# Kernel tuning notes

Hardware: AMD Instinct MI355X
Metric: run time of the kernel (lower is better)

## Reference

```python
import math
import jax, jax.numpy as jnp
import numpy as np

EPS = 1e-5

def lstm(x, Wih, Whh, b):
    # x: [N,T,D]; PyTorch gate order i,f,g,o; b = b_ih + b_hh combined
    N = x.shape[0]
    H = Whh.shape[1]
    gx = jnp.einsum('ntd,gd->ntg', x, Wih) + b  # [N,T,4H]
    def step(carry, g):
        h, c = carry
        z = g + h @ Whh.T
        i, f, gg, o = jnp.split(z, 4, axis=-1)
        c = jax.nn.sigmoid(f) * c + jax.nn.sigmoid(i) * jnp.tanh(gg)
        h = jax.nn.sigmoid(o) * jnp.tanh(c)
        return (h, c), h
    init = (jnp.zeros((N, H), x.dtype), jnp.zeros((N, H), x.dtype))
    (hN, _), ys = jax.lax.scan(step, init, jnp.swapaxes(gx, 0, 1))
    return jnp.swapaxes(ys, 0, 1), hN  # outputs [N,T,H], h_n [N,H]

def bilstm_layer(x, fW, fU, fb, bW, bU, bb):
    of, _ = lstm(x, fW, fU, fb)
    ob, _ = lstm(x[:, ::-1], bW, bU, bb)
    return jnp.concatenate([of, ob[:, ::-1]], axis=-1)

def layernorm(x, g, b):
    m = jnp.mean(x, -1, keepdims=True)
    v = jnp.mean((x - m) ** 2, -1, keepdims=True)
    return (x - m) * jax.lax.rsqrt(v + EPS) * g + b

def encoder_layer(src, Wq, bq, Wk, bk, Wv, bv, Wo, bo, W1, b1, W2, b2, lng, lnb):
    B, S, d = src.shape
    G, NH = 5, 5
    dk = d // NH
    # group channel shuffle (as in source)
    qs = src.reshape(B, S, G, d // G).swapaxes(-1, -2).reshape(B, S, d)
    q = qs @ Wq.T + bq
    k = q @ Wk.T + bk   # NOTE: source applies W_k/W_v to the projected query
    v = q @ Wv.T + bv
    def heads(t):
        return t.reshape(B, S, NH, dk).transpose(0, 2, 1, 3)
    qh, kh, vh = heads(q), heads(k), heads(v)
    attn = jax.nn.softmax(jnp.einsum('bhqd,bhkd->bhqk', qh, kh) / math.sqrt(dk), axis=-1)
    o = jnp.einsum('bhqk,bhkd->bhqd', attn, vh).transpose(0, 2, 1, 3).reshape(B, S, d)
    o = o @ Wo.T + bo
    src = layernorm(src + o, lng, lnb)          # dropout is identity in eval
    ff = jax.nn.relu(src @ W1.T + b1) @ W2.T + b2
    src = layernorm(src + ff, lng, lnb)         # same LayerNorm params reused
    return src, attn

def _forward(x, qWih, qWhh, qb, kWih, kWhh, kb, vWih, vWhh, vb,
             tWq, tbq, tWk, tbk, tWv, tbv, tWo, tbo, tW1, tb1, tW2, tb2, tlng, tlnb,
             l0fWih, l0fWhh, l0fb, l0bWih, l0bWhh, l0bb,
             l1fWih, l1fWhh, l1fb, l1bWih, l1bWhh, l1bb,
             fc1W, fc1b, fc2W, fc2b):
    B, T, F = x.shape
    H = qWhh.shape[1]
    # per-feature LSTMs: shared weights across features -> batch them
    xf = x.transpose(0, 2, 1).reshape(B * F, T, 1)
    _, hq = lstm(xf, qWih, qWhh, qb)   # [B*F,H]
    _, hk = lstm(xf, kWih, kWhh, kb)   # [B*F,H]
    _, hv = lstm(xf, vWih, vWhh, vb)   # [B*F,1]
    Q = hq.reshape(B, F, H)
    K = hk.reshape(B, F, H)
    V = hv.reshape(B, F)
    # b_ij = (q_i . k_j)/sqrt(H) * v_j, softmax over j
    scores = jnp.einsum('bih,bjh->bij', Q, K) / math.sqrt(H) * V[:, None, :]
    Wsm = jax.nn.softmax(scores, axis=-1)          # [B,F,F] rows indexed by i
    attn_output = jnp.einsum('btj,bij->bti', x, Wsm)  # bmm(x, softmax_b_i)
    b = Wsm.transpose(0, 2, 1)                     # stack(b_list, dim=-1)
    src = jnp.concatenate([x, attn_output], axis=-1)  # [B,T,2F]
    attns = []
    for l in range(2):
        src, a = encoder_layer(src, tWq[l], tbq[l], tWk[l], tbk[l], tWv[l], tbv[l],
                               tWo[l], tbo[l], tW1[l], tb1[l], tW2[l], tb2[l],
                               tlng[l], tlnb[l])
        attns.append(a)
    c = jnp.stack(attns)                           # [2,B,5,T,T]
    out = bilstm_layer(src, l0fWih, l0fWhh, l0fb, l0bWih, l0bWhh, l0bb)
    out = bilstm_layer(out, l1fWih, l1fWhh, l1fb, l1bWih, l1bWhh, l1bb)
    out = jax.nn.relu(out[:, -1, :])               # [B,2H]
    out = jax.nn.relu(out @ fc1W.T + fc1b)
    out = out @ fc2W.T + fc2b                      # [B,1]
    return out, b, c

def setup_inputs() -> dict:
    B, T, F, H = 16, 128, 40, 64
    d = 2 * F
    key = jax.random.key(0)
    ks = iter(jax.random.split(key, 64))
    def n(shape, fan):
        return (jax.random.normal(next(ks), shape) / math.sqrt(fan)).astype(jnp.float32)
    inp = {'x': jax.random.normal(next(ks), (B, T, F), dtype=jnp.float32)}
    # per-feature LSTMs
    inp.update(qWih=n((4 * H, 1), 1), qWhh=n((4 * H, H), H), qb=n((4 * H,), H))
    inp.update(kWih=n((4 * H, 1), 1), kWhh=n((4 * H, H), H), kb=n((4 * H,), H))
    inp.update(vWih=n((4, 1), 1), vWhh=n((4, 1), 1), vb=n((4,), 1))
    # transformer (2 layers stacked on leading axis)
    inp.update(tWq=n((2, d, d), d), tbq=n((2, d), d), tWk=n((2, d, d), d), tbk=n((2, d), d),
               tWv=n((2, d, d), d), tbv=n((2, d), d), tWo=n((2, d, d), d), tbo=n((2, d), d),
               tW1=n((2, 4 * d, d), d), tb1=n((2, 4 * d), d), tW2=n((2, d, 4 * d), 4 * d),
               tb2=n((2, d), 4 * d), tlng=jnp.ones((2, d), jnp.float32), tlnb=jnp.zeros((2, d), jnp.float32))
    # main bidirectional 2-layer LSTM
    inp.update(l0fWih=n((4 * H, d), d), l0fWhh=n((4 * H, H), H), l0fb=n((4 * H,), H),
               l0bWih=n((4 * H, d), d), l0bWhh=n((4 * H, H), H), l0bb=n((4 * H,), H),
               l1fWih=n((4 * H, 2 * H), 2 * H), l1fWhh=n((4 * H, H), H), l1fb=n((4 * H,), H),
               l1bWih=n((4 * H, 2 * H), 2 * H), l1bWhh=n((4 * H, H), H), l1bb=n((4 * H,), H))
    inp.update(fc1W=n((H, 2 * H), 2 * H), fc1b=n((H,), 2 * H), fc2W=n((1, H), H), fc2b=n((1,), H))
    return inp

def reference(x, qWih, qWhh, qb, kWih, kWhh, kb, vWih, vWhh, vb,
              tWq, tbq, tWk, tbk, tWv, tbv, tWo, tbo, tW1, tb1, tW2, tb2, tlng, tlnb,
              l0fWih, l0fWhh, l0fb, l0bWih, l0bWhh, l0bb,
              l1fWih, l1fWhh, l1fb, l1bWih, l1bWhh, l1bb,
              fc1W, fc1b, fc2W, fc2b):
    return _forward(x, qWih, qWhh, qb, kWih, kWhh, kb, vWih, vWhh, vb,
                    tWq, tbq, tWk, tbk, tWv, tbv, tWo, tbo, tW1, tb1, tW2, tb2, tlng, tlnb,
                    l0fWih, l0fWhh, l0fb, l0bWih, l0bWhh, l0bb,
                    l1fWih, l1fWhh, l1fb, l1bWih, l1bWhh, l1bb,
                    fc1W, fc1b, fc2W, fc2b)
```

## Files before the change

kernel.cpp:

```cpp
#include <hip/hip_runtime.h>

__device__ __forceinline__ float sigf(float x){ return 1.0f/(1.0f+__expf(-x)); }
__device__ __forceinline__ float tanhfast(float x){ return 1.0f - 2.0f/(__expf(2.0f*x)+1.0f); }

#define Bn 16
#define Tn 128
#define Fn 40
#define Hn 64
#define Dn 80
#define NHn 5
#define DKn 16
#define FFn 320

#define LOAD_PIN_ROW(dst, srcp)                                        \
  {                                                                    \
    _Pragma("unroll")                                                  \
    for (int jj=0; jj<16; ++jj){                                       \
      float4 tv = *(const float4*)((srcp) + 4*jj);                     \
      dst[4*jj]=tv.x; dst[4*jj+1]=tv.y; dst[4*jj+2]=tv.z; dst[4*jj+3]=tv.w; \
    }                                                                  \
    _Pragma("unroll")                                                  \
    for (int jj=0; jj<64; ++jj){ asm volatile("" : "+v"(dst[jj])); }   \
  }

#define LD4(p,i) (((const float4*)(p))[i])
#define DECL8(v, p) \
  float4 v##0=LD4(p,0), v##1=LD4(p,1), v##2=LD4(p,2), v##3=LD4(p,3), \
         v##4=LD4(p,4), v##5=LD4(p,5), v##6=LD4(p,6), v##7=LD4(p,7);
#define PIN4(P) asm volatile("" : "+v"(P.x), "+v"(P.y), "+v"(P.z), "+v"(P.w));
#define PIN8(v) PIN4(v##0) PIN4(v##1) PIN4(v##2) PIN4(v##3) PIN4(v##4) PIN4(v##5) \
  PIN4(v##6) PIN4(v##7)
#define ACC8(base) \
  { const float4 h0=hb4[(base)+0]; a += h0.x*w0.x + h0.y*w0.y + h0.z*w0.z + h0.w*w0.w; } \
  { const float4 h1=hb4[(base)+1]; a += h1.x*w1.x + h1.y*w1.y + h1.z*w1.z + h1.w*w1.w; } \
  { const float4 h2=hb4[(base)+2]; a += h2.x*w2.x + h2.y*w2.y + h2.z*w2.z + h2.w*w2.w; } \
  { const float4 h3=hb4[(base)+3]; a += h3.x*w3.x + h3.y*w3.y + h3.z*w3.z + h3.w*w3.w; } \
  { const float4 h4=hb4[(base)+4]; a += h4.x*w4.x + h4.y*w4.y + h4.z*w4.z + h4.w*w4.w; } \
  { const float4 h5=hb4[(base)+5]; a += h5.x*w5.x + h5.y*w5.y + h5.z*w5.z + h5.w*w5.w; } \
  { const float4 h6=hb4[(base)+6]; a += h6.x*w6.x + h6.y*w6.y + h6.z*w6.z + h6.w*w6.w; } \
  { const float4 h7=hb4[(base)+7]; a += h7.x*w7.x + h7.y*w7.y + h7.z*w7.z + h7.w*w7.w; }

__global__ __launch_bounds__(128,1) void k_feat_lstm2(
    const float* __restrict__ x,
    const float* __restrict__ qWih, const float* __restrict__ qWhh, const float* __restrict__ qb,
    const float* __restrict__ kWih, const float* __restrict__ kWhh, const float* __restrict__ kb,
    const float* __restrict__ vWih, const float* __restrict__ vWhh, const float* __restrict__ vb,
    float* __restrict__ hq, float* __restrict__ hk, float* __restrict__ hv)
{
  const int blk = blockIdx.x;
  const int l = threadIdx.x;
  if (blk >= 1280){
    const int inst = (blk - 1280)*128 + l;
    const int bi = inst/Fn, f = inst%Fn;
    const float* xp = x + bi*Tn*Fn + f;
    const float wih0=vWih[0], wih1=vWih[1], wih2=vWih[2], wih3=vWih[3];
    const float u0=vWhh[0], u1=vWhh[1], u2=vWhh[2], u3=vWhh[3];
    const float c0=vb[0], c1=vb[1], c2=vb[2], c3=vb[3];
    float h=0.f, c=0.f;
    #pragma unroll 1
    for (int t=0;t<Tn;++t){
      float xt = xp[t*Fn];
      float zi = xt*wih0 + h*u0 + c0;
      float zf = xt*wih1 + h*u1 + c1;
      float zg = xt*wih2 + h*u2 + c2;
      float zo = xt*wih3 + h*u3 + c3;
      c = sigf(zf)*c + sigf(zi)*tanhfast(zg);
      h = sigf(zo)*tanhfast(c);
    }
    hv[inst] = h;
    return;
  }
  const bool isk = blk >= 640;
  const int inst = isk ? blk-640 : blk;
  const int bi = inst/Fn, f = inst%Fn;
  const float* Whh = isk ? kWhh : qWhh;
  const float* Wih = isk ? kWih : qWih;
  const float* bia = isk ? kb  : qb;
  float* outp = isk ? hk : hq;

  const int r0 = l;
  const int r1 = l + 128;

  float w0[Hn], w1[Hn];
  LOAD_PIN_ROW(w0, Whh + r0*Hn);
  LOAD_PIN_ROW(w1, Whh + r1*Hn);
  const float wih0 = Wih[r0], wih1 = Wih[r1];
  const float bb0 = bia[r0], bb1 = bia[r1];

  __shared__ __align__(16) float hb[Hn];
  __shared__ float zb[4*Hn];
  __shared__ float xls[Tn];

  const float* xp = x + bi*Tn*Fn + f;
  xls[l] = xp[l*Fn];
  if (l < Hn) hb[l] = 0.f;
  float c = 0.f, h = 0.f;
  __syncthreads();

  const float4* hb4 = (const float4*)hb;
  #pragma unroll 1
  for (int t=0;t<Tn;++t){
    const float xt = xls[t];
    float a0 = bb0 + xt*wih0;
    float a1 = bb1 + xt*wih1;
    #pragma unroll
    for (int jj=0; jj<16; ++jj){
      const float4 hv4 = hb4[jj];
      a0 += hv4.x*w0[4*jj  ] + hv4.y*w0[4*jj+1] + hv4.z*w0[4*jj+2] + hv4.w*w0[4*jj+3];
      a1 += hv4.x*w1[4*jj  ] + hv4.y*w1[4*jj+1] + hv4.z*w1[4*jj+2] + hv4.w*w1[4*jj+3];
    }
    if (l >= Hn){ zb[l] = a0; zb[l+128] = a1; }
    __syncthreads();
    if (l < Hn){
      const float zi = a0, zg = a1;
      const float zf = zb[l+64], zo = zb[l+192];
      c = sigf(zf)*c + sigf(zi)*tanhfast(zg);
      h = sigf(zo)*tanhfast(c);
      hb[l] = h;
    }
    __syncthreads();
  }
  if (l < Hn) outp[inst*Hn + l] = h;
}

__global__ __launch_bounds__(64) void k_featattn(
    const float* __restrict__ hq, const float* __restrict__ hk, const float* __restrict__ hv,
    float* __restrict__ Wsm, float* __restrict__ out_b)
{
  const int blk = blockIdx.x;
  const int bi = blk / Fn, i = blk % Fn;
  const int j = threadIdx.x;
  __shared__ float qrow[Hn];
  qrow[j] = hq[blk*Hn + j];
  __syncthreads();
  float s = -1e30f;
  if (j < Fn){
    const float* krow = hk + (bi*Fn + j)*Hn;
    float a = 0.f;
    #pragma unroll
    for (int h2=0; h2<Hn; ++h2) a += qrow[h2]*krow[h2];
    s = a * 0.125f * hv[bi*Fn + j];
  }
  float m = s;
  #pragma unroll
  for (int off=32; off>0; off>>=1) m = fmaxf(m, __shfl_xor(m, off));
  float e = (j < Fn) ? __expf(s - m) : 0.f;
  float tot = e;
  #pragma unroll
  for (int off=32; off>0; off>>=1) tot += __shfl_xor(tot, off);
  float p = e / tot;
  if (j < Fn){
    Wsm[blk*Fn + j] = p;
    out_b[bi*(Fn*Fn) + j*Fn + i] = p;
  }
}

__global__ __launch_bounds__(128) void k_build_src(
    const float* __restrict__ x, const float* __restrict__ Wsm, float* __restrict__ src)
{
  const int blk = blockIdx.x;
  const int bi = blk / Tn;
  const int tid = threadIdx.x;
  __shared__ float xrow[Fn];
  if (tid < Fn) xrow[tid] = x[blk*Fn + tid];
  __syncthreads();
  if (tid < Fn){
    src[blk*Dn + tid] = xrow[tid];
  } else if (tid < Dn){
    const int i = tid - Fn;
    const float* wrow = Wsm + (bi*Fn + i)*Fn;
    float a = 0.f;
    #pragma unroll
    for (int j2=0;j2<Fn;++j2) a += xrow[j2]*wrow[j2];
    src[blk*Dn + tid] = a;
  }
}

__global__ __launch_bounds__(128) void k_qkv(
    const float* __restrict__ src,
    const float* __restrict__ Wq, const float* __restrict__ bq,
    const float* __restrict__ Wk, const float* __restrict__ bk,
    const float* __restrict__ Wv, const float* __restrict__ bv,
    float* __restrict__ q, float* __restrict__ k, float* __restrict__ v)
{
  const int row = blockIdx.x;
  const int t = threadIdx.x;
  __shared__ float qs[Dn];
  __shared__ float qrow[Dn];
  if (t < Dn) qs[t] = src[row*Dn + (t%5)*16 + t/5];
  __syncthreads();
  if (t < Dn){
    const float* wr = Wq + t*Dn;
    float a = bq[t];
    #pragma unroll 8
    for (int d2=0; d2<Dn; ++d2) a += qs[d2]*wr[d2];
    qrow[t] = a;
    q[row*Dn + t] = a;
  }
  __syncthreads();
  if (t < Dn){
    const float* wk = Wk + t*Dn;
    const float* wv = Wv + t*Dn;
    float ak = bk[t], av = bv[t];
    #pragma unroll 8
    for (int d2=0; d2<Dn; ++d2){ float qq = qrow[d2]; ak += qq*wk[d2]; av += qq*wv[d2]; }
    k[row*Dn + t] = ak;
    v[row*Dn + t] = av;
  }
}

__global__ __launch_bounds__(128) void k_attn(
    const float* __restrict__ q, const float* __restrict__ k, const float* __restrict__ v,
    float* __restrict__ o, float* __restrict__ c_out)
{
  const int s1 = blockIdx.x, h = blockIdx.y, bi = blockIdx.z;
  const int s2 = threadIdx.x;
  __shared__ float qf[DKn];
  __shared__ float p[Tn];
  __shared__ float pa[128];
  __shared__ float red_m[2];
  __shared__ float red_s[2];
  if (s2 < DKn) qf[s2] = q[(bi*Tn + s1)*Dn + h*DKn + s2];
  __syncthreads();
  const float* krow = k + (bi*Tn + s2)*Dn + h*DKn;
  float a = 0.f;
  #pragma unroll
  for (int d2=0; d2<DKn; ++d2) a += qf[d2]*krow[d2];
  a *= 0.25f;
  const int wv_id = s2 >> 6;
  float m = a;
  #pragma unroll
  for (int off=32; off>0; off>>=1) m = fmaxf(m, __shfl_xor(m, off));
  if ((s2 & 63) == 0) red_m[wv_id] = m;
  __syncthreads();
  m = fmaxf(red_m[0], red_m[1]);
  float e = __expf(a - m);
  float tot = e;
  #pragma unroll
  for (int off=32; off>0; off>>=1) tot += __shfl_xor(tot, off);
  if ((s2 & 63) == 0) red_s[wv_id] = tot;
  __syncthreads();
  tot = red_s[0] + red_s[1];
  float pv = e / tot;
  p[s2] = pv;
  c_out[((bi*NHn + h)*Tn + s1)*Tn + s2] = pv;
  __syncthreads();
  {
    const int d    = s2 & 15;
    const int part = s2 >> 4;
    const float* vcol = v + bi*Tn*Dn + h*DKn + d;
    float acc = 0.f;
    #pragma unroll
    for (int jj=0; jj<16; ++jj){
      const int j2 = part*16 + jj;
      acc += p[j2]*vcol[j2*Dn];
    }
    pa[s2] = acc;
  }
  __syncthreads();
  if (s2 < DKn){
    float acc = 0.f;
    #pragma unroll
    for (int k2=0; k2<8; ++k2) acc += pa[k2*16 + s2];
    o[(bi*Tn + s1)*Dn + h*DKn + s2] = acc;
  }
}

__global__ __launch_bounds__(320) void k_oln_ffln(
    const float* __restrict__ o, const float* __restrict__ Wo, const float* __restrict__ bo,
    const float* __restrict__ W1, const float* __restrict__ b1,
    const float* __restrict__ W2, const float* __restrict__ b2,
    const float* __restrict__ lng, const float* __restrict__ lnb, float* __restrict__ src)
{
  const int row = blockIdx.x;
  const int t = threadIdx.x;
  __shared__ float orow[Dn];
  __shared__ float s1row[Dn];
  __shared__ float h1[FFn];
  __shared__ float red[128];
  if (t < Dn) orow[t] = o[row*Dn + t];
  __syncthreads();
  float val = 0.f;
  if (t < Dn){
    const float* wr = Wo + t*Dn;
    float a = bo[t];
    #pragma unroll 8
    for (int d2=0; d2<Dn; ++d2) a += orow[d2]*wr[d2];
    val = a + src[row*Dn + t];
  }
  if (t < 128) red[t] = (t < Dn) ? val : 0.f;
  __syncthreads();
  for (int s=64; s>0; s>>=1){ if (t < s) red[t] += red[t+s]; __syncthreads(); }
  float mean = red[0] * (1.f/Dn);
  __syncthreads();
  if (t < 128){ float dv = (t < Dn) ? (val - mean) : 0.f; red[t] = dv*dv; }
  __syncthreads();
  for (int s=64; s>0; s>>=1){ if (t < s) red[t] += red[t+s]; __syncthreads(); }
  float rstd = rsqrtf(red[0]*(1.f/Dn) + 1e-5f);
  if (t < Dn) s1row[t] = (val - mean)*rstd*lng[t] + lnb[t];
  __syncthreads();
  {
    const float* wr = W1 + t*Dn;
    float a = b1[t];
    #pragma unroll 8
    for (int d2=0; d2<Dn; ++d2) a += s1row[d2]*wr[d2];
    h1[t] = fmaxf(a, 0.f);
  }
  __syncthreads();
  float val2 = 0.f;
  if (t < Dn){
    const float* wr = W2 + t*FFn;
    float a = b2[t];
    #pragma unroll 8
    for (int d2=0; d2<FFn; ++d2) a += h1[d2]*wr[d2];
    val2 = a + s1row[t];
  }
  if (t < 128) red[t] = (t < Dn) ? val2 : 0.f;
  __syncthreads();
  for (int s=64; s>0; s>>=1){ if (t < s) red[t] += red[t+s]; __syncthreads(); }
  mean = red[0] * (1.f/Dn);
  __syncthreads();
  if (t < 128){ float dv = (t < Dn) ? (val2 - mean) : 0.f; red[t] = dv*dv; }
  __syncthreads();
  for (int s=64; s>0; s>>=1){ if (t < s) red[t] += red[t+s]; __syncthreads(); }
  rstd = rsqrtf(red[0]*(1.f/Dn) + 1e-5f);
  if (t < Dn) src[row*Dn + t] = (val2 - mean)*rstd*lng[t] + lnb[t];
}

template<int IND>
__global__ __launch_bounds__(256) void k_gx8(
    const float* __restrict__ X,
    const float* __restrict__ WihF, const float* __restrict__ bF,
    const float* __restrict__ WihB, const float* __restrict__ bB,
    float* __restrict__ gx)
{
  const int row0 = blockIdx.x * 8;
  const int dir = blockIdx.y;
  const int g = threadIdx.x;
  __shared__ float xs[8][IND];
  #pragma unroll
  for (int rr=0; rr<8; ++rr)
    for (int d2=g; d2<IND; d2+=256) xs[rr][d2] = X[(row0+rr)*IND + d2];
  __syncthreads();
  const float* W  = dir ? WihB : WihF;
  const float* bb = dir ? bB  : bF;
  const float* wr = W + g*IND;
  float acc[8];
  const float b0 = bb[g];
  #pragma unroll
  for (int rr=0; rr<8; ++rr) acc[rr] = b0;
  #pragma unroll 4
  for (int d2=0; d2<IND; d2+=4){
    const float4 wv = *(const float4*)(wr + d2);
    #pragma unroll
    for (int rr=0; rr<8; ++rr){
      acc[rr] += xs[rr][d2]*wv.x + xs[rr][d2+1]*wv.y + xs[rr][d2+2]*wv.z + xs[rr][d2+3]*wv.w;
    }
  }
  float* gxd = gx + dir*(Bn*Tn*256);
  #pragma unroll
  for (int rr=0; rr<8; ++rr) gxd[(row0+rr)*256 + g] = acc[rr];
}

__global__ __launch_bounds__(512)
void k_bilstm_rec5(
    const float* __restrict__ gx,
    const float* __restrict__ WhhF, const float* __restrict__ WhhB,
    float* __restrict__ outp)
{
  const int n = blockIdx.x;
  const int dir = blockIdx.y;
  const int t = threadIdx.x;
  const int half = t >> 8;
  const int r    = t & 255;
  const float* Whh = dir ? WhhB : WhhF;
  DECL8(w, Whh + r*Hn + half*32);
  PIN8(w);

  __shared__ __align__(16) float hb[Hn];
  __shared__ float pa[512];
  if (t < Hn) hb[t] = 0.f;
  float c = 0.f, h = 0.f;
  __syncthreads();

  const float* gxd = gx + dir*(Bn*Tn*256) + n*Tn*256;
  const float4* hb4 = (const float4*)hb;
  const int jbase = half*8;
  const int t0 = dir ? Tn-1 : 0;
  float g0 = half ? 0.f : gxd[t0*256 + r];
  #pragma unroll 1
  for (int step=0; step<Tn; ++step){
    const int tt = dir ? (Tn-1-step) : step;
    int tn = dir ? (Tn-2-step) : (step+1);
    tn = max(0, min(Tn-1, tn));
    const float p0 = half ? 0.f : gxd[tn*256 + r];
    float a = g0;
    ACC8(jbase)
    pa[t] = a;
    __syncthreads();
    if (t < Hn){
      const float zi = pa[t    ] + pa[t+256];
      const float zf = pa[t+ 64] + pa[t+320];
      const float zg = pa[t+128] + pa[t+384];
      const float zo = pa[t+192] + pa[t+448];
      c = sigf(zf)*c + sigf(zi)*tanhfast(zg);
      h = sigf(zo)*tanhfast(c);
      hb[t] = h;
      outp[(n*Tn + tt)*128 + dir*Hn + t] = h;
    }
    __syncthreads();
    g0 = p0;
  }
}

__global__ __launch_bounds__(128) void k_final(
    const float* __restrict__ out1,
    const float* __restrict__ fc1W, const float* __restrict__ fc1b,
    const float* __restrict__ fc2W, const float* __restrict__ fc2b,
    float* __restrict__ outp)
{
  const int n = blockIdx.x;
  const int t = threadIdx.x;
  __shared__ float r[128];
  __shared__ float a1[64];
  r[t] = fmaxf(out1[(n*Tn + (Tn-1))*128 + t], 0.f);
  __syncthreads();
  if (t < 64){
    const float* wr = fc1W + t*128;
    float a = fc1b[t];
    #pragma unroll 8
    for (int d2=0; d2<128; ++d2) a += r[d2]*wr[d2];
    a1[t] = fmaxf(a, 0.f);
  }
  __syncthreads();
  if (t == 0){
    float a = fc2b[0];
    #pragma unroll 8
    for (int d2=0; d2<64; ++d2) a += a1[d2]*fc2W[d2];
    outp[n] = a;
  }
}

extern "C" void kernel_launch(void* const* d_in, const int* in_sizes, int n_in,
                              void* d_out, int out_size, void* d_ws, size_t ws_size,
                              hipStream_t stream)
{
  const float* x     = (const float*)d_in[0];
  const float* qWih  = (const float*)d_in[1];
  const float* qWhh  = (const float*)d_in[2];
  const float* qb    = (const float*)d_in[3];
  const float* kWih  = (const float*)d_in[4];
  const float* kWhh  = (const float*)d_in[5];
  const float* kb    = (const float*)d_in[6];
  const float* vWih  = (const float*)d_in[7];
  const float* vWhh  = (const float*)d_in[8];
  const float* vb    = (const float*)d_in[9];
  const float* tWq   = (const float*)d_in[10];
  const float* tbq   = (const float*)d_in[11];
  const float* tWk   = (const float*)d_in[12];
  const float* tbk   = (const float*)d_in[13];
  const float* tWv   = (const float*)d_in[14];
  const float* tbv   = (const float*)d_in[15];
  const float* tWo   = (const float*)d_in[16];
  const float* tbo   = (const float*)d_in[17];
  const float* tW1   = (const float*)d_in[18];
  const float* tb1   = (const float*)d_in[19];
  const float* tW2   = (const float*)d_in[20];
  const float* tb2   = (const float*)d_in[21];
  const float* tlng  = (const float*)d_in[22];
  const float* tlnb  = (const float*)d_in[23];
  const float* l0fWih= (const float*)d_in[24];
  const float* l0fWhh= (const float*)d_in[25];
  const float* l0fb  = (const float*)d_in[26];
  const float* l0bWih= (const float*)d_in[27];
  const float* l0bWhh= (const float*)d_in[28];
  const float* l0bb  = (const float*)d_in[29];
  const float* l1fWih= (const float*)d_in[30];
  const float* l1fWhh= (const float*)d_in[31];
  const float* l1fb  = (const float*)d_in[32];
  const float* l1bWih= (const float*)d_in[33];
  const float* l1bWhh= (const float*)d_in[34];
  const float* l1bb  = (const float*)d_in[35];
  const float* fc1W  = (const float*)d_in[36];
  const float* fc1b  = (const float*)d_in[37];
  const float* fc2W  = (const float*)d_in[38];
  const float* fc2b  = (const float*)d_in[39];

  float* ws  = (float*)d_ws;
  float* hq  = ws;
  float* hk  = hq  + 640*64;
  float* hv  = hk  + 640*64;
  float* Wsm = hv  + 640;
  float* src = Wsm + 16*40*40;
  float* q   = src + 16*128*80;
  float* k   = q   + 16*128*80;
  float* v   = k   + 16*128*80;
  float* o   = v   + 16*128*80;
  float* gx  = o   + 16*128*80;
  float* lout0 = gx + 2*16*128*256;
  float* lout1 = lout0 + 16*128*128;

  float* outp  = (float*)d_out;
  float* out_b = outp + 16;
  float* out_c = out_b + 16*40*40;

  k_feat_lstm2<<<1285, 128, 0, stream>>>(x, qWih,qWhh,qb, kWih,kWhh,kb, vWih,vWhh,vb, hq,hk,hv);
  k_featattn<<<640, 64, 0, stream>>>(hq, hk, hv, Wsm, out_b);
  k_build_src<<<2048, 128, 0, stream>>>(x, Wsm, src);
  for (int l=0; l<2; ++l){
    k_qkv<<<2048, 128, 0, stream>>>(src, tWq + l*Dn*Dn, tbq + l*Dn,
                                    tWk + l*Dn*Dn, tbk + l*Dn,
                                    tWv + l*Dn*Dn, tbv + l*Dn, q, k, v);
    k_attn<<<dim3(128,5,16), 128, 0, stream>>>(q, k, v, o, out_c + (size_t)l*16*5*128*128);
    k_oln_ffln<<<2048, 320, 0, stream>>>(o, tWo + l*Dn*Dn, tbo + l*Dn,
                                         tW1 + l*FFn*Dn, tb1 + l*FFn,
                                         tW2 + l*Dn*FFn, tb2 + l*Dn,
                                         tlng + l*Dn, tlnb + l*Dn, src);
  }
  k_gx8<80><<<dim3(256,2), 256, 0, stream>>>(src, l0fWih, l0fb, l0bWih, l0bb, gx);
  k_bilstm_rec5<<<dim3(16,2), 512, 0, stream>>>(gx, l0fWhh, l0bWhh, lout0);
  k_gx8<128><<<dim3(256,2), 256, 0, stream>>>(lout0, l1fWih, l1fb, l1bWih, l1bb, gx);
  k_bilstm_rec5<<<dim3(16,2), 512, 0, stream>>>(gx, l1fWhh, l1bWhh, lout1);
  k_final<<<16, 128, 0, stream>>>(lout1, fc1W, fc1b, fc2W, fc2b, outp);
}
```

Baseline: 665.3 us.

## Use one gate row per thread in feature LSTM with 256-thread blocks

The per-feature LSTM kernel now uses 256 threads per block, each holding one 64-wide Whh row in registers instead of two. All gate pre-activations go through shared memory, and the dot product is split into two accumulators for more instruction-level parallelism. Launch bounds allow five blocks per CU, cutting register pressure and raising occupancy. The scalar v-LSTM tail now packs 256 instances per block. The trade-off is twice as many threads taking part in each step's barriers.

```diff
diff --git a/kernel.cpp b/kernel.cpp
--- a/kernel.cpp
+++ b/kernel.cpp
@@ -11,17 +11,6 @@
 #define NHn 5
 #define DKn 16
 #define FFn 320
-
-#define LOAD_PIN_ROW(dst, srcp)                                        \
-  {                                                                    \
-    _Pragma("unroll")                                                  \
-    for (int jj=0; jj<16; ++jj){                                       \
-      float4 tv = *(const float4*)((srcp) + 4*jj);                     \
-      dst[4*jj]=tv.x; dst[4*jj+1]=tv.y; dst[4*jj+2]=tv.z; dst[4*jj+3]=tv.w; \
-    }                                                                  \
-    _Pragma("unroll")                                                  \
-    for (int jj=0; jj<64; ++jj){ asm volatile("" : "+v"(dst[jj])); }   \
-  }
 
 #define LD4(p,i) (((const float4*)(p))[i])
 #define DECL8(v, p) \
@@ -40,7 +29,15 @@
   { const float4 h6=hb4[(base)+6]; a += h6.x*w6.x + h6.y*w6.y + h6.z*w6.z + h6.w*w6.w; } \
   { const float4 h7=hb4[(base)+7]; a += h7.x*w7.x + h7.y*w7.y + h7.z*w7.z + h7.w*w7.w; }
 
-__global__ __launch_bounds__(128,1) void k_feat_lstm2(
+#define CAT_(a,b) a##b
+#define CAT(a,b) CAT_(a,b)
+#define ACC1P(v, n, idx, acc) \
+  { const float4 hh=hb4[(idx)]; acc += hh.x*CAT(v,n).x + hh.y*CAT(v,n).y + hh.z*CAT(v,n).z + hh.w*CAT(v,n).w; }
+#define ACC8P(v, base, acc) \
+  ACC1P(v,0,(base)+0,acc) ACC1P(v,1,(base)+1,acc) ACC1P(v,2,(base)+2,acc) ACC1P(v,3,(base)+3,acc) \
+  ACC1P(v,4,(base)+4,acc) ACC1P(v,5,(base)+5,acc) ACC1P(v,6,(base)+6,acc) ACC1P(v,7,(base)+7,acc)
+
+__global__ __launch_bounds__(256,5) void k_feat_lstm2(
     const float* __restrict__ x,
     const float* __restrict__ qWih, const float* __restrict__ qWhh, const float* __restrict__ qb,
     const float* __restrict__ kWih, const float* __restrict__ kWhh, const float* __restrict__ kb,
@@ -50,7 +47,8 @@
   const int blk = blockIdx.x;
   const int l = threadIdx.x;
   if (blk >= 1280){
-    const int inst = (blk - 1280)*128 + l;
+    const int inst = (blk - 1280)*256 + l;
+    if (inst >= 640) return;
     const int bi = inst/Fn, f = inst%Fn;
     const float* xp = x + bi*Tn*Fn + f;
     const float wih0=vWih[0], wih1=vWih[1], wih2=vWih[2], wih3=vWih[3];
@@ -78,21 +76,19 @@
   const float* bia = isk ? kb  : qb;
   float* outp = isk ? hk : hq;
 
-  const int r0 = l;
-  const int r1 = l + 128;
-
-  float w0[Hn], w1[Hn];
-  LOAD_PIN_ROW(w0, Whh + r0*Hn);
-  LOAD_PIN_ROW(w1, Whh + r1*Hn);
-  const float wih0 = Wih[r0], wih1 = Wih[r1];
-  const float bb0 = bia[r0], bb1 = bia[r1];
+  const float* wr = Whh + l*Hn;
+  DECL8(wA, wr);
+  DECL8(wB, wr + 32);
+  PIN8(wA); PIN8(wB);
+  const float wih0 = Wih[l];
+  const float bb0  = bia[l];
 
   __shared__ __align__(16) float hb[Hn];
-  __shared__ float zb[4*Hn];
+  __shared__ float zb[256];
   __shared__ float xls[Tn];
 
   const float* xp = x + bi*Tn*Fn + f;
-  xls[l] = xp[l*Fn];
+  if (l < Tn) xls[l] = xp[l*Fn];
   if (l < Hn) hb[l] = 0.f;
   float c = 0.f, h = 0.f;
   __syncthreads();
@@ -101,19 +97,14 @@
   #pragma unroll 1
   for (int t=0;t<Tn;++t){
     const float xt = xls[t];
-    float a0 = bb0 + xt*wih0;
-    float a1 = bb1 + xt*wih1;
-    #pragma unroll
-    for (int jj=0; jj<16; ++jj){
-      const float4 hv4 = hb4[jj];
-      a0 += hv4.x*w0[4*jj  ] + hv4.y*w0[4*jj+1] + hv4.z*w0[4*jj+2] + hv4.w*w0[4*jj+3];
-      a1 += hv4.x*w1[4*jj  ] + hv4.y*w1[4*jj+1] + hv4.z*w1[4*jj+2] + hv4.w*w1[4*jj+3];
-    }
-    if (l >= Hn){ zb[l] = a0; zb[l+128] = a1; }
+    float a  = bb0 + xt*wih0;
+    float a2 = 0.f;
+    ACC8P(wA, 0, a)
+    ACC8P(wB, 8, a2)
+    zb[l] = a + a2;
     __syncthreads();
     if (l < Hn){
-      const float zi = a0, zg = a1;
-      const float zf = zb[l+64], zo = zb[l+192];
+      const float zi = zb[l], zf = zb[l+64], zg = zb[l+128], zo = zb[l+192];
       c = sigf(zf)*c + sigf(zi)*tanhfast(zg);
       h = sigf(zo)*tanhfast(c);
       hb[l] = h;
@@ -504,7 +495,7 @@
   float* out_b = outp + 16;
   float* out_c = out_b + 16*40*40;
 
-  k_feat_lstm2<<<1285, 128, 0, stream>>>(x, qWih,qWhh,qb, kWih,kWhh,kb, vWih,vWhh,vb, hq,hk,hv);
+  k_feat_lstm2<<<1283, 256, 0, stream>>>(x, qWih,qWhh,qb, kWih,kWhh,kb, vWih,vWhh,vb, hq,hk,hv);
   k_featattn<<<640, 64, 0, stream>>>(hq, hk, hv, Wsm, out_b);
   k_build_src<<<2048, 128, 0, stream>>>(x, Wsm, src);
   for (int l=0; l<2; ++l){
```

Result: slower. 705.6 us (+6.1%).
